# Optimization experiments

Measured on AMD Instinct MI355X. Metric: run time of the kernel, lower is better.

## Reference

```python
import jax, jax.numpy as jnp
import numpy as np

# --- configuration (mirrors init_kwargs) ---
N_G = (256, 256, 128, 128)   # tem.hyper['n_g'] per-module sizes
N_ACTIONS = 4                 # tem action space
NUM_STATES = 4096
BATCH = 16384
G_TOTAL = sum(N_G)            # 768


def setup_inputs() -> dict:
    key = jax.random.key(0)
    ks = jax.random.split(key, 4 + len(N_G))
    inp = {
        "current_state_index": jax.random.randint(ks[0], (BATCH,), 0, NUM_STATES),
        "action_index": jax.random.randint(ks[1], (BATCH,), 0, N_ACTIONS),
        # xavier-ish init scale for embedding / classifier
        "emb": jax.random.normal(ks[2], (NUM_STATES, G_TOTAL), jnp.float32) * 0.02,
        "W_cls": jax.random.normal(ks[3], (NUM_STATES, G_TOTAL), jnp.float32) * 0.02,
        "b_cls": jnp.zeros((NUM_STATES,), jnp.float32),
    }
    # per-module bank of action-conditioned transition matrices D_a: [n_actions, n_g_f, n_g_f]
    for f, n in enumerate(N_G):
        inp[f"D{f}"] = jax.random.normal(ks[4 + f], (N_ACTIONS, n, n), jnp.float32) * (1.0 / np.sqrt(n))
    return inp


def _transition(g_f, D_f, onehot):
    # Routed action-conditioned transition (replaces the CPU per-action loop):
    # delta[b, j] = sum_i D_f[a_b, j, i] * g_f[b, i], dispatched via one-hot over actions.
    delta = jnp.einsum('aji,bi,ba->bj', D_f, g_f, onehot)
    # TEM generative clamp activation f_g_clamp
    return jnp.clip(g_f + delta, -1.0, 1.0)


def reference(current_state_index, action_index, emb, D0, D1, D2, D3, W_cls, b_cls):
    g_flat = emb[current_state_index]                                   # [B, G_TOTAL]
    onehot = jax.nn.one_hot(action_index, N_ACTIONS, dtype=g_flat.dtype)  # [B, A]
    # _split_g: slice flat grid code into TEM modules
    g_mods = jnp.split(g_flat, np.cumsum(np.array(N_G))[:-1].tolist(), axis=1)
    Ds = (D0, D1, D2, D3)
    g_next = [_transition(g_f, D_f, onehot) for g_f, D_f in zip(g_mods, Ds)]
    g_next_flat = jnp.concatenate(g_next, axis=1)                       # [B, G_TOTAL]
    logits = g_next_flat @ W_cls.T + b_cls                              # [B, NUM_STATES]
    return logits, g_next_flat
```

## Files before the change

### kernel.cpp

```cpp
#include <hip/hip_runtime.h>
#include <hip/hip_bf16.h>
#include <stdint.h>


typedef __attribute__((ext_vector_type(8))) short short8;
typedef __attribute__((ext_vector_type(4))) float floatx4;

__device__ __forceinline__ float bf2f(short s) {
    unsigned int u = ((unsigned int)(unsigned short)s) << 16;
    float f;
    __builtin_memcpy(&f, &u, 4);
    return f;
}
__device__ __forceinline__ short f2bf(float f) {
    unsigned int u;
    __builtin_memcpy(&u, &f, 4);
    u = (u + 0x7FFFu + ((u >> 16) & 1u)) >> 16;
    return (short)u;
}

#define GLLDS16(g, l)                                                                     \
    __builtin_amdgcn_global_load_lds((const __attribute__((address_space(1))) void*)(g),  \
                                     (__attribute__((address_space(3))) void*)(l), 16, 0, 0)

#define ROWS_PAD 16896

__global__ __launch_bounds__(1024) void setup_kernel(const int* __restrict__ act,
                                                     int* __restrict__ meta,
                                                     int* __restrict__ s2o) {
    const int tid = threadIdx.x;
    const int lane = tid & 63;
    const int w = tid >> 6;
    __shared__ int lc[16][4];
    int c0 = 0, c1 = 0, c2 = 0, c3 = 0;
    for (int i = tid; i < 16384; i += 1024) {
        int a = act[i];
        unsigned long long m0 = __ballot(a == 0);
        unsigned long long m1 = __ballot(a == 1);
        unsigned long long m2 = __ballot(a == 2);
        unsigned long long m3 = __ballot(a == 3);
        if (lane == 0) {
            c0 += __popcll(m0); c1 += __popcll(m1);
            c2 += __popcll(m2); c3 += __popcll(m3);
        }
    }
    if (lane == 0) { lc[w][0] = c0; lc[w][1] = c1; lc[w][2] = c2; lc[w][3] = c3; }
    for (int i = tid; i < ROWS_PAD; i += 1024) s2o[i] = -1;
    __syncthreads();
    if (tid == 0) {
        int base = 0;
        for (int k = 0; k < 4; ++k) {
            int c = 0;
            for (int ww = 0; ww < 16; ++ww) c += lc[ww][k];
            meta[4 + k] = base;
            meta[9 + k] = base;
            base += (c + 127) & ~127;
        }
        meta[8] = base;
    }
}

__global__ __launch_bounds__(256) void assign_kernel(const int* __restrict__ act,
                                                     int* __restrict__ meta,
                                                     int* __restrict__ slot_of,
                                                     int* __restrict__ s2o) {
    const int row = blockIdx.x * 256 + threadIdx.x;
    const int lane = threadIdx.x & 63;
    const int a = act[row];
    const unsigned long long lt = (1ull << lane) - 1ull;
    int* cursor = meta + 9;
    int slot = 0;
    #pragma unroll
    for (int k = 0; k < 4; ++k) {
        unsigned long long m = __ballot(a == k);
        int c = __popcll(m);
        int gb = 0;
        if (lane == 0 && c) gb = atomicAdd(&cursor[k], c);
        gb = __shfl(gb, 0);
        if (a == k) slot = gb + __popcll(m & lt);
    }
    slot_of[row] = slot;
    s2o[slot] = row;
}

__global__ __launch_bounds__(256) void prep_kernel(
    const int* __restrict__ state, const int* __restrict__ slot_of,
    const float* __restrict__ emb, const float* __restrict__ W,
    const float* __restrict__ D0, const float* __restrict__ D1,
    const float* __restrict__ D2, const float* __restrict__ D3,
    short* __restrict__ A1, short* __restrict__ Wb, short* __restrict__ Db) {
    long e = (long)blockIdx.x * 256 + threadIdx.x;
    const float* src;
    short* dst;
    long di;
    if (e < 3145728L) {
        int b = (int)(e / 192);
        int cc = (int)(e % 192);
        int s = state[b];
        int d = slot_of[b];
        src = emb + (long)s * 768 + cc * 4;
        dst = A1; di = (long)d * 192 + cc;
    } else if (e < 3932160L) {
        long t = e - 3145728L;
        src = W + t * 4; dst = Wb; di = t;
    } else if (e < 3997696L) {
        long t = e - 3932160L;
        src = D0 + t * 4; dst = Db; di = t;
    } else if (e < 4063232L) {
        long t = e - 3997696L;
        src = D1 + t * 4; dst = Db + 262144; di = t;
    } else if (e < 4079616L) {
        long t = e - 4063232L;
        src = D2 + t * 4; dst = Db + 524288; di = t;
    } else {
        long t = e - 4079616L;
        src = D3 + t * 4; dst = Db + 589824; di = t;
    }
    float4 v = *(const float4*)src;
    union { ushort4 u4; short s4[4]; } o;
    o.s4[0] = f2bf(v.x); o.s4[1] = f2bf(v.y);
    o.s4[2] = f2bf(v.z); o.s4[3] = f2bf(v.w);
    *(ushort4*)(dst + di * 4) = o.u4;
}

__global__ __launch_bounds__(256) void trans_gemm_kernel(
    const short* __restrict__ A, const short* __restrict__ Db,
    const int* __restrict__ meta, const int* __restrict__ s2o,
    float* __restrict__ gnext, short* __restrict__ A2) {
    __shared__ short Ash[128 * 64];
    __shared__ short Bsh[128 * 64];
    const int bx = blockIdx.x, bm = blockIdx.y;
    int n, bn, coloff;
    long Doff;
    if (bx < 4) {
        n = 256; bn = bx & 1;
        int f = bx >> 1;
        coloff = f * 256; Doff = (long)f * 262144;
    } else {
        n = 128; bn = 0;
        int f = bx - 4;
        coloff = 512 + f * 128; Doff = 524288 + (long)f * 65536;
    }
    const int rowbase = bm * 128;
    const int sb4 = meta[8];
    if (rowbase >= sb4) return;
    const int a = (rowbase >= meta[5]) + (rowbase >= meta[6]) + (rowbase >= meta[7]);
    const short* Bm = Db + Doff + (long)a * n * n;

    const int tid = threadIdx.x;
    const int lane = tid & 63;
    const int w = tid >> 6;
    const int wm = w & 1, wn = w >> 1;
    const long arow0 = (long)rowbase;
    const long brow0 = (long)bn * 128;
    const int lrow = lane & 15;
    const int q = lane >> 4;

    floatx4 acc[4][4] = {};

    for (int k0 = 0; k0 < n; k0 += 64) {
        #pragma unroll
        for (int it = 0; it < 4; ++it) {
            int c = it * 256 + tid;
            int r = c >> 3, cc = c & 7;
            int gc = cc ^ (r & 7);
            GLLDS16(A + (arow0 + r) * 768 + coloff + k0 + gc * 8, &Ash[c * 8]);
            GLLDS16(Bm + (brow0 + r) * n + k0 + gc * 8, &Bsh[c * 8]);
        }
        __syncthreads();
        #pragma unroll
        for (int kk = 0; kk < 2; ++kk) {
            short8 af[4], bv[4];
            #pragma unroll
            for (int mi = 0; mi < 4; ++mi) {
                int rr = wm * 64 + mi * 16 + lrow;
                int ch = (kk * 4 + q) ^ (rr & 7);
                af[mi] = *(const short8*)&Ash[rr * 64 + ch * 8];
            }
            #pragma unroll
            for (int ni = 0; ni < 4; ++ni) {
                int rr = wn * 64 + ni * 16 + lrow;
                int ch = (kk * 4 + q) ^ (rr & 7);
                bv[ni] = *(const short8*)&Bsh[rr * 64 + ch * 8];
            }
            #pragma unroll
            for (int mi = 0; mi < 4; ++mi)
                #pragma unroll
                for (int ni = 0; ni < 4; ++ni)
                    acc[mi][ni] = __builtin_amdgcn_mfma_f32_16x16x32_bf16(
                        af[mi], bv[ni], acc[mi][ni], 0, 0, 0);
        }
        __syncthreads();
    }

    const int jb = bn * 128 + wn * 64;
    const int rowb2 = rowbase + wm * 64;
    #pragma unroll
    for (int mi = 0; mi < 4; ++mi) {
        #pragma unroll
        for (int r = 0; r < 4; ++r) {
            int srow = rowb2 + mi * 16 + q * 4 + r;
            int orig = s2o[srow];
            if (orig >= 0) {
                #pragma unroll
                for (int ni = 0; ni < 4; ++ni) {
                    int jl = jb + ni * 16 + lrow;
                    long sidx = (long)srow * 768 + coloff + jl;
                    float g = bf2f(A[sidx]);
                    float v = g + acc[mi][ni][r];
                    v = fminf(1.0f, fmaxf(-1.0f, v));
                    gnext[(long)orig * 768 + coloff + jl] = v;
                    A2[sidx] = f2bf(v);
                }
            }
        }
    }
}

__global__ __launch_bounds__(256) void cls_gemm_kernel(
    const short* __restrict__ A, const short* __restrict__ Bm,
    const float* __restrict__ bias, const int* __restrict__ meta,
    const int* __restrict__ s2o, float* __restrict__ out) {
    __shared__ short Ash[128 * 64];
    __shared__ short Bsh[128 * 64];
    const int bn = blockIdx.x, bm = blockIdx.y;
    const int rowbase = bm * 128;
    if (rowbase >= meta[8]) return;
    const int tid = threadIdx.x;
    const int lane = tid & 63;
    const int w = tid >> 6;
    const int wm = w & 1, wn = w >> 1;
    const long arow0 = (long)rowbase;
    const long brow0 = (long)bn * 128;
    const int lrow = lane & 15;
    const int q = lane >> 4;

    floatx4 acc[4][4] = {};

    for (int k0 = 0; k0 < 768; k0 += 64) {
        #pragma unroll
        for (int it = 0; it < 4; ++it) {
            int c = it * 256 + tid;
            int r = c >> 3, cc = c & 7;
            int gc = cc ^ (r & 7);
            GLLDS16(A + (arow0 + r) * 768 + k0 + gc * 8, &Ash[c * 8]);
            GLLDS16(Bm + (brow0 + r) * 768 + k0 + gc * 8, &Bsh[c * 8]);
        }
        __syncthreads();
        #pragma unroll
        for (int kk = 0; kk < 2; ++kk) {
            short8 af[4], bv[4];
            #pragma unroll
            for (int mi = 0; mi < 4; ++mi) {
                int rr = wm * 64 + mi * 16 + lrow;
                int ch = (kk * 4 + q) ^ (rr & 7);
                af[mi] = *(const short8*)&Ash[rr * 64 + ch * 8];
            }
            #pragma unroll
            for (int ni = 0; ni < 4; ++ni) {
                int rr = wn * 64 + ni * 16 + lrow;
                int ch = (kk * 4 + q) ^ (rr & 7);
                bv[ni] = *(const short8*)&Bsh[rr * 64 + ch * 8];
            }
            #pragma unroll
            for (int mi = 0; mi < 4; ++mi)
                #pragma unroll
                for (int ni = 0; ni < 4; ++ni)
                    acc[mi][ni] = __builtin_amdgcn_mfma_f32_16x16x32_bf16(
                        af[mi], bv[ni], acc[mi][ni], 0, 0, 0);
        }
        __syncthreads();
    }

    const int rowb2 = rowbase + wm * 64;
    const int colbase = bn * 128 + wn * 64;
    #pragma unroll
    for (int mi = 0; mi < 4; ++mi) {
        #pragma unroll
        for (int r = 0; r < 4; ++r) {
            int srow = rowb2 + mi * 16 + q * 4 + r;
            int orig = s2o[srow];
            if (orig >= 0) {
                #pragma unroll
                for (int ni = 0; ni < 4; ++ni) {
                    int col = colbase + ni * 16 + lrow;
                    out[(long)orig * 4096 + col] = acc[mi][ni][r] + bias[col];
                }
            }
        }
    }
}

extern "C" void kernel_launch(void* const* d_in, const int* in_sizes, int n_in,
                              void* d_out, int out_size, void* d_ws, size_t ws_size,
                              hipStream_t stream) {
    const int* state  = (const int*)d_in[0];
    const int* act    = (const int*)d_in[1];
    const float* emb  = (const float*)d_in[2];
    const float* W    = (const float*)d_in[3];
    const float* bias = (const float*)d_in[4];
    const float* D0   = (const float*)d_in[5];
    const float* D1   = (const float*)d_in[6];
    const float* D2   = (const float*)d_in[7];
    const float* D3   = (const float*)d_in[8];

    float* logits = (float*)d_out;
    float* gnext  = logits + 67108864L;

    short* A1 = (short*)d_ws;
    short* A2 = A1 + 12976128L;
    short* Wb = A2 + 12976128L;
    short* Db = Wb + 3145728L;
    int* meta    = (int*)(Db + 655360);
    int* slot_of = meta + 16;
    int* s2o     = slot_of + 16384;

    setup_kernel<<<1, 1024, 0, stream>>>(act, meta, s2o);
    assign_kernel<<<64, 256, 0, stream>>>(act, meta, slot_of, s2o);
    prep_kernel<<<16000, 256, 0, stream>>>(state, slot_of, emb, W, D0, D1, D2, D3,
                                           A1, Wb, Db);
    trans_gemm_kernel<<<dim3(6, 132), 256, 0, stream>>>(A1, Db, meta, s2o, gnext, A2);
    cls_gemm_kernel<<<dim3(32, 132), 256, 0, stream>>>(A2, Wb, bias, meta, s2o, logits);
}
```

Before: 565.9 us.

## Pipeline classifier GEMM with 4-stage LDS ring and 256x256 tiles

Reworks the classifier GEMM to use 256x256 output tiles with 512 threads, a four-buffer LDS ring of BK=32 slices fed by async global-to-LDS loads, and vmcnt-based waits so loads overlap MFMA compute with one barrier per step. It also remaps block indices for L2 locality and raises MFMA wave priority during compute. The intent is to hide memory latency and raise operand reuse in this GEMM. The cost is more registers per thread (8x4 accumulators) and 128KB of LDS, which limits occupancy, plus fragile hand-counted vmcnt values.

```diff
diff --git a/kernel.cpp b/kernel.cpp
--- a/kernel.cpp
+++ b/kernel.cpp
@@ -217,65 +217,86 @@
     }
 }
 
-__global__ __launch_bounds__(256) void cls_gemm_kernel(
+__global__ __launch_bounds__(512) void cls_gemm_kernel(
     const short* __restrict__ A, const short* __restrict__ Bm,
     const float* __restrict__ bias, const int* __restrict__ meta,
     const int* __restrict__ s2o, float* __restrict__ out) {
-    __shared__ short Ash[128 * 64];
-    __shared__ short Bsh[128 * 64];
-    const int bn = blockIdx.x, bm = blockIdx.y;
-    const int rowbase = bm * 128;
+    __shared__ short lds[4][2][8192];
+
+    int lin = blockIdx.y * 16 + blockIdx.x;
+    lin = (lin & 7) * 132 + (lin >> 3);
+    const int bn = lin & 15, bm = lin >> 4;
+    const int rowbase = bm * 256;
     if (rowbase >= meta[8]) return;
+
     const int tid = threadIdx.x;
     const int lane = tid & 63;
     const int w = tid >> 6;
     const int wm = w & 1, wn = w >> 1;
     const long arow0 = (long)rowbase;
-    const long brow0 = (long)bn * 128;
+    const long brow0 = (long)bn * 256;
     const int lrow = lane & 15;
     const int q = lane >> 4;
 
-    floatx4 acc[4][4] = {};
-
-    for (int k0 = 0; k0 < 768; k0 += 64) {
-        #pragma unroll
-        for (int it = 0; it < 4; ++it) {
-            int c = it * 256 + tid;
-            int r = c >> 3, cc = c & 7;
-            int gc = cc ^ (r & 7);
-            GLLDS16(A + (arow0 + r) * 768 + k0 + gc * 8, &Ash[c * 8]);
-            GLLDS16(Bm + (brow0 + r) * 768 + k0 + gc * 8, &Bsh[c * 8]);
-        }
-        __syncthreads();
-        #pragma unroll
-        for (int kk = 0; kk < 2; ++kk) {
-            short8 af[4], bv[4];
+    floatx4 acc[8][4] = {};
+
+    auto STAGE = [&](int t, int b) {
+        const int k0 = t * 32;
+        #pragma unroll
+        for (int it = 0; it < 2; ++it) {
+            int c = it * 512 + tid;
+            int r = c >> 2, s = c & 3;
+            int gc = s ^ ((r >> 1) & 3);
+            GLLDS16(A + (arow0 + r) * 768 + k0 + gc * 8, &lds[b][0][c * 8]);
+            GLLDS16(Bm + (brow0 + r) * 768 + k0 + gc * 8, &lds[b][1][c * 8]);
+        }
+    };
+
+    auto COMPUTE = [&](int b) {
+        const short* Ab = lds[b][0];
+        const short* Bb = lds[b][1];
+        short8 af[8], bv[4];
+        #pragma unroll
+        for (int mi = 0; mi < 8; ++mi) {
+            int rr = wm * 128 + mi * 16 + lrow;
+            int sl = q ^ ((rr >> 1) & 3);
+            af[mi] = *(const short8*)&Ab[rr * 32 + sl * 8];
+        }
+        #pragma unroll
+        for (int ni = 0; ni < 4; ++ni) {
+            int rr = wn * 64 + ni * 16 + lrow;
+            int sl = q ^ ((rr >> 1) & 3);
+            bv[ni] = *(const short8*)&Bb[rr * 32 + sl * 8];
+        }
+        __builtin_amdgcn_s_setprio(1);
+        #pragma unroll
+        for (int mi = 0; mi < 8; ++mi)
             #pragma unroll
-            for (int mi = 0; mi < 4; ++mi) {
-                int rr = wm * 64 + mi * 16 + lrow;
-                int ch = (kk * 4 + q) ^ (rr & 7);
-                af[mi] = *(const short8*)&Ash[rr * 64 + ch * 8];
-            }
-            #pragma unroll
-            for (int ni = 0; ni < 4; ++ni) {
-                int rr = wn * 64 + ni * 16 + lrow;
-                int ch = (kk * 4 + q) ^ (rr & 7);
-                bv[ni] = *(const short8*)&Bsh[rr * 64 + ch * 8];
-            }
-            #pragma unroll
-            for (int mi = 0; mi < 4; ++mi)
-                #pragma unroll
-                for (int ni = 0; ni < 4; ++ni)
-                    acc[mi][ni] = __builtin_amdgcn_mfma_f32_16x16x32_bf16(
-                        af[mi], bv[ni], acc[mi][ni], 0, 0, 0);
-        }
-        __syncthreads();
-    }
-
-    const int rowb2 = rowbase + wm * 64;
-    const int colbase = bn * 128 + wn * 64;
+            for (int ni = 0; ni < 4; ++ni)
+                acc[mi][ni] = __builtin_amdgcn_mfma_f32_16x16x32_bf16(
+                    af[mi], bv[ni], acc[mi][ni], 0, 0, 0);
+        __builtin_amdgcn_s_setprio(0);
+    };
+
+    STAGE(0, 0); STAGE(1, 1); STAGE(2, 2);
+
+    for (int t = 0; t < 22; ++t) {
+        asm volatile("s_waitcnt vmcnt(8)" ::: "memory");
+        __builtin_amdgcn_s_barrier();
+        if (t < 21) STAGE(t + 3, (t + 3) & 3);
+        COMPUTE(t & 3);
+    }
+    asm volatile("s_waitcnt vmcnt(4)" ::: "memory");
+    __builtin_amdgcn_s_barrier();
+    COMPUTE(22 & 3);
+    asm volatile("s_waitcnt vmcnt(0)" ::: "memory");
+    __builtin_amdgcn_s_barrier();
+    COMPUTE(23 & 3);
+
+    const int rowb2 = rowbase + wm * 128;
+    const int colbase = bn * 256 + wn * 64;
     #pragma unroll
-    for (int mi = 0; mi < 4; ++mi) {
+    for (int mi = 0; mi < 8; ++mi) {
         #pragma unroll
         for (int r = 0; r < 4; ++r) {
             int srow = rowb2 + mi * 16 + q * 4 + r;
@@ -320,5 +341,5 @@
     prep_kernel<<<16000, 256, 0, stream>>>(state, slot_of, emb, W, D0, D1, D2, D3,
                                            A1, Wb, Db);
     trans_gemm_kernel<<<dim3(6, 132), 256, 0, stream>>>(A1, Db, meta, s2o, gnext, A2);
-    cls_gemm_kernel<<<dim3(32, 132), 256, 0, stream>>>(A2, Wb, bias, meta, s2o, logits);
-}
+    cls_gemm_kernel<<<dim3(16, 66), 512, 0, stream>>>(A2, Wb, bias, meta, s2o, logits);
+}
```

Result: faster. 527.3 us (-6.8%).
